# Kernel tuning notes

Measured on AMD Instinct MI355X. Metric: run time of the kernel, lower is better.

Reference implementation:

```python
import jax, jax.numpy as jnp
import numpy as np

B, T, D, H = 2, 2048, 1024, 16  # batch, seq, n_embed, n_head


def setup_inputs() -> dict:
    key = jax.random.key(0)
    ks = jax.random.split(key, 5)
    scale = 1.0 / np.sqrt(D)
    return {
        "x": jax.random.normal(ks[0], (B, T, D), dtype=jnp.float32),
        "Wq": jax.random.normal(ks[1], (D, D), dtype=jnp.float32) * scale,
        "Wk": jax.random.normal(ks[2], (D, D), dtype=jnp.float32) * scale,
        "Wv": jax.random.normal(ks[3], (D, D), dtype=jnp.float32) * scale,
        "Wo": jax.random.normal(ks[4], (D, D), dtype=jnp.float32) * scale,
    }


def reference(x, Wq, Wk, Wv, Wo):
    b, t, d = x.shape
    hd = d // H  # head_dim
    # projections -> [B, H, T, hd]
    q = (x @ Wq).reshape(b, t, H, hd).transpose(0, 2, 1, 3)
    k = (x @ Wk).reshape(b, t, H, hd).transpose(0, 2, 1, 3)
    v = (x @ Wv).reshape(b, t, H, hd).transpose(0, 2, 1, 3)
    # scaled scores [B, H, T, T] with causal mask
    e = jnp.einsum("bhqd,bhkd->bhqk", q, k) * (1.0 / np.sqrt(hd))
    causal = jnp.tril(jnp.ones((t, t), dtype=bool))
    e = jnp.where(causal[None, None], e, jnp.finfo(e.dtype).min)
    alpha = jax.nn.softmax(e, axis=-1)
    # attention output -> [B, T, D]
    attn = jnp.einsum("bhqk,bhkd->bhqd", alpha, v)
    attn = attn.transpose(0, 2, 1, 3).reshape(b, t, d)
    return attn @ Wo
```

## Files before the change

### kernel.cpp

```cpp
#include <hip/hip_runtime.h>
#include <hip/hip_bf16.h>
#include <math.h>


#define Bsz  2
#define Tseq 2048
#define Dm   1024
#define NH   16
#define HD   64

typedef short bf16x8 __attribute__((ext_vector_type(8)));
typedef float floatx4 __attribute__((ext_vector_type(4)));

__device__ __forceinline__ unsigned short f2bf(float f) {
    __hip_bfloat16 h = __float2bfloat16(f);
    return *reinterpret_cast<unsigned short*>(&h);
}

__device__ __forceinline__ unsigned short f2bf_fast(float f) {
    unsigned int u = __builtin_bit_cast(unsigned int, f);
    return (unsigned short)((u + 0x8000u) >> 16);
}

__device__ __forceinline__ void lds16(unsigned short* lds, const unsigned short* g) {
    __builtin_amdgcn_global_load_lds(
        (const __attribute__((address_space(1))) void*)g,
        (__attribute__((address_space(3))) void*)lds, 16, 0, 0);
}

__global__ __launch_bounds__(256) void prep(const float* __restrict__ x,
                                            const float* __restrict__ W0,
                                            const float* __restrict__ W1,
                                            const float* __restrict__ W2,
                                            const float* __restrict__ W3,
                                            unsigned short* __restrict__ xb,
                                            unsigned short* __restrict__ T0,
                                            unsigned short* __restrict__ T1,
                                            unsigned short* __restrict__ T2,
                                            unsigned short* __restrict__ T3) {
    __shared__ float t[64][65];
    const int z = blockIdx.z;
    if (z >= 4) {
        const int bi = (z - 4) * 256 + blockIdx.y * 16 + blockIdx.x;
        const size_t i = (size_t)bi * 256 + threadIdx.x;
        const float4 v = ((const float4*)x)[i];
        ushort4 o;
        o.x = f2bf(v.x); o.y = f2bf(v.y); o.z = f2bf(v.z); o.w = f2bf(v.w);
        ((ushort4*)xb)[i] = o;
        return;
    }
    const float* W = (z == 0) ? W0 : (z == 1) ? W1 : (z == 2) ? W2 : W3;
    unsigned short* T = (z == 0) ? T0 : (z == 1) ? T1 : (z == 2) ? T2 : T3;
    const int k0 = blockIdx.y * 64, n0 = blockIdx.x * 64;
    const int row = threadIdx.x >> 6, col = threadIdx.x & 63;
#pragma unroll
    for (int p = 0; p < 16; ++p)
        t[p * 4 + row][col] = W[(size_t)(k0 + p * 4 + row) * Dm + n0 + col];
    __syncthreads();
#pragma unroll
    for (int p = 0; p < 16; ++p)
        T[(size_t)(n0 + p * 4 + row) * Dm + k0 + col] = f2bf(t[col][p * 4 + row]);
}

__device__ __forceinline__ void gemm128_mainloop(const unsigned short* __restrict__ A,
                                                 const unsigned short* __restrict__ Bt,
                                                 int K, int m0, int n0,
                                                 unsigned short* As, unsigned short* Bs,
                                                 floatx4 acc[4][4]) {
    const int tid = threadIdx.x;
    const int lane = tid & 63, wave = tid >> 6;
    const int l15 = lane & 15, quad = lane >> 4;
    const int wm = (wave >> 1) * 64, wn = (wave & 1) * 64;

    const int qsw = (quad ^ ((l15 >> 1) & 3)) * 8;

    for (int k0 = 0; k0 < K; k0 += 32) {
        __syncthreads();
#pragma unroll
        for (int c = 0; c < 2; ++c) {
            const int idx = c * 256 + tid;
            const int row = idx >> 2, kc = (idx & 3) * 8;
            const int sk = ((idx & 3) ^ ((row >> 1) & 3)) * 8;
            lds16(&As[row * 32 + kc], A + (size_t)(m0 + row) * K + k0 + sk);
            lds16(&Bs[row * 32 + kc], Bt + (size_t)(n0 + row) * K + k0 + sk);
        }
        __syncthreads();
        bf16x8 af[4], bfr[4];
#pragma unroll
        for (int i = 0; i < 4; ++i)
            af[i] = *(const bf16x8*)&As[(wm + i * 16 + l15) * 32 + qsw];
#pragma unroll
        for (int j = 0; j < 4; ++j)
            bfr[j] = *(const bf16x8*)&Bs[(wn + j * 16 + l15) * 32 + qsw];
#pragma unroll
        for (int i = 0; i < 4; ++i)
#pragma unroll
            for (int j = 0; j < 4; ++j)
                acc[i][j] = __builtin_amdgcn_mfma_f32_16x16x32_bf16(af[i], bfr[j], acc[i][j], 0, 0, 0);
    }
}

__global__ __launch_bounds__(256) void gemm_qkv(const unsigned short* __restrict__ xb,
                                                const unsigned short* __restrict__ Wqt,
                                                const unsigned short* __restrict__ Wkt,
                                                const unsigned short* __restrict__ Wvt,
                                                unsigned short* __restrict__ Qb,
                                                unsigned short* __restrict__ Kb,
                                                unsigned short* __restrict__ VbT) {
    __shared__ unsigned short As[128 * 32];
    __shared__ unsigned short Bs[128 * 32];
    const int z = blockIdx.z;
    const unsigned short* Bt = (z == 0) ? Wqt : (z == 1) ? Wkt : Wvt;
    const float scale = (z == 0) ? (0.125f * 1.4426950408889634f) : 1.0f;
    const int m0 = blockIdx.y * 128, n0 = blockIdx.x * 128;

    floatx4 acc[4][4];
#pragma unroll
    for (int i = 0; i < 4; ++i)
#pragma unroll
        for (int j = 0; j < 4; ++j) acc[i][j] = (floatx4){0.f, 0.f, 0.f, 0.f};

    gemm128_mainloop(xb, Bt, Dm, m0, n0, As, Bs, acc);

    const int lane = threadIdx.x & 63, wave = threadIdx.x >> 6;
    const int l15 = lane & 15, quad = lane >> 4;
    const int wm = (wave >> 1) * 64, wn = (wave & 1) * 64;

    if (z == 2) {
#pragma unroll
        for (int i = 0; i < 4; ++i)
#pragma unroll
            for (int j = 0; j < 4; ++j) {
                const int col = n0 + wn + j * 16 + l15;
                const int hh = col >> 6, dd = col & 63;
                const int tok = m0 + wm + i * 16 + quad * 4;
                const int bb = tok >> 11, tl = tok & (Tseq - 1);
                ushort4 o;
                o.x = f2bf(acc[i][j][0]); o.y = f2bf(acc[i][j][1]);
                o.z = f2bf(acc[i][j][2]); o.w = f2bf(acc[i][j][3]);
                *(ushort4*)&VbT[((size_t)((bb * NH + hh) * HD + dd)) * Tseq + tl] = o;
            }
        return;
    }
    unsigned short* C = (z == 0) ? Qb : Kb;
#pragma unroll
    for (int i = 0; i < 4; ++i)
#pragma unroll
        for (int j = 0; j < 4; ++j)
#pragma unroll
            for (int r = 0; r < 4; ++r) {
                const int row = m0 + wm + i * 16 + quad * 4 + r;
                const int col = n0 + wn + j * 16 + l15;
                C[(size_t)row * Dm + col] = f2bf(acc[i][j][r] * scale);
            }
}

__global__ __launch_bounds__(256) void gemm_out(const unsigned short* __restrict__ Yb,
                                                const unsigned short* __restrict__ Wot,
                                                float* __restrict__ out) {
    __shared__ unsigned short As[128 * 32];
    __shared__ unsigned short Bs[64 * 32];
    const int m0 = blockIdx.y * 128, n0 = blockIdx.x * 64;
    const int tid = threadIdx.x;
    const int lane = tid & 63, wave = tid >> 6;
    const int l15 = lane & 15, quad = lane >> 4;
    const int wm = (wave >> 1) * 64, wn = (wave & 1) * 32;
    const int qsw = (quad ^ ((l15 >> 1) & 3)) * 8;

    floatx4 acc[4][2];
#pragma unroll
    for (int i = 0; i < 4; ++i)
#pragma unroll
        for (int j = 0; j < 2; ++j) acc[i][j] = (floatx4){0.f, 0.f, 0.f, 0.f};

    for (int k0 = 0; k0 < Dm; k0 += 32) {
        __syncthreads();
#pragma unroll
        for (int c = 0; c < 2; ++c) {
            const int idx = c * 256 + tid;
            const int row = idx >> 2, kc = (idx & 3) * 8;
            const int sk = ((idx & 3) ^ ((row >> 1) & 3)) * 8;
            lds16(&As[row * 32 + kc], Yb + (size_t)(m0 + row) * Dm + k0 + sk);
        }
        {
            const int row = tid >> 2, kc = (tid & 3) * 8;
            const int sk = ((tid & 3) ^ ((row >> 1) & 3)) * 8;
            lds16(&Bs[row * 32 + kc], Wot + (size_t)(n0 + row) * Dm + k0 + sk);
        }
        __syncthreads();
        bf16x8 af[4], bfr[2];
#pragma unroll
        for (int i = 0; i < 4; ++i)
            af[i] = *(const bf16x8*)&As[(wm + i * 16 + l15) * 32 + qsw];
#pragma unroll
        for (int j = 0; j < 2; ++j)
            bfr[j] = *(const bf16x8*)&Bs[(wn + j * 16 + l15) * 32 + qsw];
#pragma unroll
        for (int i = 0; i < 4; ++i)
#pragma unroll
            for (int j = 0; j < 2; ++j)
                acc[i][j] = __builtin_amdgcn_mfma_f32_16x16x32_bf16(af[i], bfr[j], acc[i][j], 0, 0, 0);
    }

#pragma unroll
    for (int i = 0; i < 4; ++i)
#pragma unroll
        for (int j = 0; j < 2; ++j)
#pragma unroll
            for (int r = 0; r < 4; ++r) {
                const int row = m0 + wm + i * 16 + quad * 4 + r;
                const int col = n0 + wn + j * 16 + l15;
                out[(size_t)row * Dm + col] = acc[i][j][r];
            }
}

__global__ __launch_bounds__(256) void attn_mfma(const unsigned short* __restrict__ Qb,
                                                 const unsigned short* __restrict__ Kb,
                                                 const unsigned short* __restrict__ VbT,
                                                 unsigned short* __restrict__ Yb) {
    const int bh = blockIdx.x;
    const int b = bh >> 4;
    const int h = bh & 15;
    const int qt = 31 - blockIdx.y;
    const int tid = threadIdx.x;
    const int wave = tid >> 6;
    const int lane = tid & 63;
    const int l15 = lane & 15;
    const int quad = lane >> 4;

    __shared__ unsigned short Ks0[2][2][64][32];
    __shared__ unsigned short Ks1[2][2][64][32];
    __shared__ unsigned short Vt0[2][2][64][32];
    __shared__ unsigned short Vt1[2][2][64][32];
    __shared__ unsigned short Ps[4][16][72];

    const size_t tok0 = (size_t)b * Tseq;
    const int colh = h * HD;
    const unsigned short* vbase = VbT + (size_t)bh * HD * Tseq;

    const int qrow = qt * 64 + wave * 16;

    const unsigned short* qptr = Qb + (tok0 + qrow + l15) * Dm + colh + quad * 8;
    const bf16x8 qf0 = *(const bf16x8*)(qptr);
    const bf16x8 qf1 = *(const bf16x8*)(qptr + 32);

    float l_lane = 0.f;
    floatx4 o_acc[4];
#pragma unroll
    for (int t = 0; t < 4; ++t) o_acc[t] = (floatx4){0.f, 0.f, 0.f, 0.f};

    const int srow = tid >> 2;
    const int sc8 = (tid & 3) * 8;
    const int ssw = ((tid & 3) ^ ((srow >> 1) & 3)) * 8;
    const int qsw = (quad ^ ((l15 >> 1) & 3)) * 8;

    const int niter = (qt + 2) >> 1;

    {
        const unsigned short* krow0 = Kb + (tok0 + srow) * Dm + colh;
        const unsigned short* krow1 = Kb + (tok0 + 64 + srow) * Dm + colh;
        const unsigned short* vrow = vbase + (size_t)srow * Tseq;
        lds16(&Ks0[0][0][srow][sc8], krow0 + ssw);
        lds16(&Ks1[0][0][srow][sc8], krow0 + 32 + ssw);
        lds16(&Vt0[0][0][srow][sc8], vrow + ssw);
        lds16(&Vt1[0][0][srow][sc8], vrow + 32 + ssw);
        lds16(&Ks0[0][1][srow][sc8], krow1 + ssw);
        lds16(&Ks1[0][1][srow][sc8], krow1 + 32 + ssw);
        lds16(&Vt0[0][1][srow][sc8], vrow + 64 + ssw);
        lds16(&Vt1[0][1][srow][sc8], vrow + 64 + 32 + ssw);
    }
    asm volatile("s_waitcnt vmcnt(0)" ::: "memory");
    __builtin_amdgcn_s_barrier();
    __builtin_amdgcn_sched_barrier(0);

    for (int it = 0; it < niter; ++it) {
        const int k0 = it * 128;
        const int bi = it & 1;

        if (it + 1 < niter) {
            const int kn = k0 + 128;
#pragma unroll
            for (int s = 0; s < 2; ++s) {
                const unsigned short* krow = Kb + (tok0 + kn + s * 64 + srow) * Dm + colh;
                const unsigned short* vrow = vbase + (size_t)srow * Tseq + kn + s * 64;
                lds16(&Ks0[bi ^ 1][s][srow][sc8], krow + ssw);
                lds16(&Ks1[bi ^ 1][s][srow][sc8], krow + 32 + ssw);
                lds16(&Vt0[bi ^ 1][s][srow][sc8], vrow + ssw);
                lds16(&Vt1[bi ^ 1][s][srow][sc8], vrow + 32 + ssw);
            }
        }
        __builtin_amdgcn_sched_barrier(0);

#pragma unroll
        for (int s = 0; s < 2; ++s) {
            const int k0s = k0 + s * 64;
            if (k0s > qrow + 15) continue;

            floatx4 sf[4];
            __builtin_amdgcn_s_setprio(1);
#pragma unroll
            for (int t = 0; t < 4; ++t) {
                floatx4 c = (floatx4){0.f, 0.f, 0.f, 0.f};
                const bf16x8 kb0 = *(const bf16x8*)&Ks0[bi][s][t * 16 + l15][qsw];
                const bf16x8 kb1 = *(const bf16x8*)&Ks1[bi][s][t * 16 + l15][qsw];
                c = __builtin_amdgcn_mfma_f32_16x16x32_bf16(kb0, qf0, c, 0, 0, 0);
                c = __builtin_amdgcn_mfma_f32_16x16x32_bf16(kb1, qf1, c, 0, 0, 0);
                sf[t] = c;
            }
            __builtin_amdgcn_s_setprio(0);

            if (k0s + 63 > qrow) {
                const int ql = qrow + l15;
#pragma unroll
                for (int t = 0; t < 4; ++t)
#pragma unroll
                    for (int r = 0; r < 4; ++r) {
                        const int kl = k0s + t * 16 + quad * 4 + r;
                        if (kl > ql) sf[t][r] = -1.0e30f;
                    }
            }

#pragma unroll
            for (int t = 0; t < 4; ++t) {
                float p0 = __builtin_amdgcn_exp2f(sf[t][0]);
                float p1 = __builtin_amdgcn_exp2f(sf[t][1]);
                float p2 = __builtin_amdgcn_exp2f(sf[t][2]);
                float p3 = __builtin_amdgcn_exp2f(sf[t][3]);
                l_lane += (p0 + p1) + (p2 + p3);
                unsigned int w0, w1;
                asm("v_cvt_pk_bf16_f32 %0, %1, %2" : "=v"(w0) : "v"(p0), "v"(p1));
                asm("v_cvt_pk_bf16_f32 %0, %1, %2" : "=v"(w1) : "v"(p2), "v"(p3));
                uint2 o; o.x = w0; o.y = w1;
                *(uint2*)&Ps[wave][l15][t * 16 + quad * 4] = o;
            }

            const bf16x8 pa0 = *(const bf16x8*)&Ps[wave][l15][quad * 8];
            const bf16x8 pa1 = *(const bf16x8*)&Ps[wave][l15][32 + quad * 8];
            __builtin_amdgcn_s_setprio(1);
#pragma unroll
            for (int t = 0; t < 4; ++t) {
                const bf16x8 vb0 = *(const bf16x8*)&Vt0[bi][s][t * 16 + l15][qsw];
                const bf16x8 vb1 = *(const bf16x8*)&Vt1[bi][s][t * 16 + l15][qsw];
                o_acc[t] = __builtin_amdgcn_mfma_f32_16x16x32_bf16(pa0, vb0, o_acc[t], 0, 0, 0);
                o_acc[t] = __builtin_amdgcn_mfma_f32_16x16x32_bf16(pa1, vb1, o_acc[t], 0, 0, 0);
            }
            __builtin_amdgcn_s_setprio(0);
        }

        asm volatile("s_waitcnt vmcnt(0)" ::: "memory");
        __builtin_amdgcn_s_barrier();
        __builtin_amdgcn_sched_barrier(0);
    }

    l_lane += __shfl_xor(l_lane, 16);
    l_lane += __shfl_xor(l_lane, 32);
    const float inv_q = 1.0f / l_lane;
    float inv_r[4];
#pragma unroll
    for (int r = 0; r < 4; ++r)
        inv_r[r] = __shfl(inv_q, (lane & 48) | (quad * 4 + r));
#pragma unroll
    for (int t = 0; t < 4; ++t)
#pragma unroll
        for (int r = 0; r < 4; ++r) {
            const int q = qrow + quad * 4 + r;
            Yb[(tok0 + q) * Dm + colh + t * 16 + l15] = f2bf(o_acc[t][r] * inv_r[r]);
        }
}

extern "C" void kernel_launch(void* const* d_in, const int* in_sizes, int n_in,
                              void* d_out, int out_size, void* d_ws, size_t ws_size,
                              hipStream_t stream) {
    const float* x  = (const float*)d_in[0];
    const float* Wq = (const float*)d_in[1];
    const float* Wk = (const float*)d_in[2];
    const float* Wv = (const float*)d_in[3];
    const float* Wo = (const float*)d_in[4];
    float* out = (float*)d_out;

    const int M = Bsz * Tseq;
    char* ws = (char*)d_ws;
    unsigned short* xb  = (unsigned short*)(ws);
    unsigned short* Wqt = (unsigned short*)(ws + (((size_t)8)  << 20));
    unsigned short* Wkt = (unsigned short*)(ws + (((size_t)10) << 20));
    unsigned short* Wvt = (unsigned short*)(ws + (((size_t)12) << 20));
    unsigned short* Wot = (unsigned short*)(ws + (((size_t)14) << 20));
    unsigned short* Qb  = (unsigned short*)(ws + (((size_t)16) << 20));
    unsigned short* Kb  = (unsigned short*)(ws + (((size_t)24) << 20));
    unsigned short* VbT = (unsigned short*)(ws + (((size_t)32) << 20));
    unsigned short* Yb  = (unsigned short*)(ws + (((size_t)40) << 20));

    dim3 blk(256);
    hipLaunchKernelGGL(prep, dim3(16, 16, 20), blk, 0, stream,
                       x, Wq, Wk, Wv, Wo, xb, Wqt, Wkt, Wvt, Wot);

    hipLaunchKernelGGL(gemm_qkv, dim3(Dm / 128, M / 128, 3), blk, 0, stream,
                       xb, Wqt, Wkt, Wvt, Qb, Kb, VbT);

    hipLaunchKernelGGL(attn_mfma, dim3(Bsz * NH, 32), blk, 0, stream, Qb, Kb, VbT, Yb);

    hipLaunchKernelGGL(gemm_out, dim3(Dm / 64, M / 128), blk, 0, stream, Yb, Wot, out);
}
```

Before: 171.8 us.

## Remap GEMM tile order and simplify attention to single-buffered 64-key tiles

```diff
diff --git a/kernel.cpp b/kernel.cpp
--- a/kernel.cpp
+++ b/kernel.cpp
@@ -112,7 +112,11 @@
     const int z = blockIdx.z;
     const unsigned short* Bt = (z == 0) ? Wqt : (z == 1) ? Wkt : Wvt;
     const float scale = (z == 0) ? (0.125f * 1.4426950408889634f) : 1.0f;
-    const int m0 = blockIdx.y * 128, n0 = blockIdx.x * 128;
+
+    const int wg = blockIdx.x + 8 * blockIdx.y;
+    const int m_idx = (wg & 7) * 4 + (wg >> 6);
+    const int n_idx = (wg >> 3) & 7;
+    const int m0 = m_idx * 128, n0 = n_idx * 128;
 
     floatx4 acc[4][4];
 #pragma unroll
@@ -160,7 +164,10 @@
                                                 float* __restrict__ out) {
     __shared__ unsigned short As[128 * 32];
     __shared__ unsigned short Bs[64 * 32];
-    const int m0 = blockIdx.y * 128, n0 = blockIdx.x * 64;
+    const int wg = blockIdx.x + 16 * blockIdx.y;
+    const int m_idx = (wg & 7) * 4 + (wg >> 7);
+    const int n_idx = (wg >> 3) & 15;
+    const int m0 = m_idx * 128, n0 = n_idx * 64;
     const int tid = threadIdx.x;
     const int lane = tid & 63, wave = tid >> 6;
     const int l15 = lane & 15, quad = lane >> 4;
@@ -228,15 +235,14 @@
     const int l15 = lane & 15;
     const int quad = lane >> 4;
 
-    __shared__ unsigned short Ks0[2][2][64][32];
-    __shared__ unsigned short Ks1[2][2][64][32];
-    __shared__ unsigned short Vt0[2][2][64][32];
-    __shared__ unsigned short Vt1[2][2][64][32];
+    __shared__ unsigned short Ks0[64][32];
+    __shared__ unsigned short Ks1[64][32];
+    __shared__ unsigned short Vt0[64][32];
+    __shared__ unsigned short Vt1[64][32];
     __shared__ unsigned short Ps[4][16][72];
 
     const size_t tok0 = (size_t)b * Tseq;
     const int colh = h * HD;
-    const unsigned short* vbase = VbT + (size_t)bh * HD * Tseq;
 
     const int qrow = qt * 64 + wave * 16;
 
@@ -254,102 +260,70 @@
     const int ssw = ((tid & 3) ^ ((srow >> 1) & 3)) * 8;
     const int qsw = (quad ^ ((l15 >> 1) & 3)) * 8;
 
-    const int niter = (qt + 2) >> 1;
-
-    {
-        const unsigned short* krow0 = Kb + (tok0 + srow) * Dm + colh;
-        const unsigned short* krow1 = Kb + (tok0 + 64 + srow) * Dm + colh;
-        const unsigned short* vrow = vbase + (size_t)srow * Tseq;
-        lds16(&Ks0[0][0][srow][sc8], krow0 + ssw);
-        lds16(&Ks1[0][0][srow][sc8], krow0 + 32 + ssw);
-        lds16(&Vt0[0][0][srow][sc8], vrow + ssw);
-        lds16(&Vt1[0][0][srow][sc8], vrow + 32 + ssw);
-        lds16(&Ks0[0][1][srow][sc8], krow1 + ssw);
-        lds16(&Ks1[0][1][srow][sc8], krow1 + 32 + ssw);
-        lds16(&Vt0[0][1][srow][sc8], vrow + 64 + ssw);
-        lds16(&Vt1[0][1][srow][sc8], vrow + 64 + 32 + ssw);
-    }
-    asm volatile("s_waitcnt vmcnt(0)" ::: "memory");
-    __builtin_amdgcn_s_barrier();
-    __builtin_amdgcn_sched_barrier(0);
-
+    const unsigned short* krow = Kb + (tok0 + srow) * Dm + colh;
+    const unsigned short* vrow = VbT + (size_t)bh * HD * Tseq + (size_t)srow * Tseq;
+
+    const int niter = qt + 1;
     for (int it = 0; it < niter; ++it) {
-        const int k0 = it * 128;
-        const int bi = it & 1;
-
-        if (it + 1 < niter) {
-            const int kn = k0 + 128;
-#pragma unroll
-            for (int s = 0; s < 2; ++s) {
-                const unsigned short* krow = Kb + (tok0 + kn + s * 64 + srow) * Dm + colh;
-                const unsigned short* vrow = vbase + (size_t)srow * Tseq + kn + s * 64;
-                lds16(&Ks0[bi ^ 1][s][srow][sc8], krow + ssw);
-                lds16(&Ks1[bi ^ 1][s][srow][sc8], krow + 32 + ssw);
-                lds16(&Vt0[bi ^ 1][s][srow][sc8], vrow + ssw);
-                lds16(&Vt1[bi ^ 1][s][srow][sc8], vrow + 32 + ssw);
-            }
-        }
-        __builtin_amdgcn_sched_barrier(0);
-
-#pragma unroll
-        for (int s = 0; s < 2; ++s) {
-            const int k0s = k0 + s * 64;
-            if (k0s > qrow + 15) continue;
-
-            floatx4 sf[4];
-            __builtin_amdgcn_s_setprio(1);
-#pragma unroll
-            for (int t = 0; t < 4; ++t) {
-                floatx4 c = (floatx4){0.f, 0.f, 0.f, 0.f};
-                const bf16x8 kb0 = *(const bf16x8*)&Ks0[bi][s][t * 16 + l15][qsw];
-                const bf16x8 kb1 = *(const bf16x8*)&Ks1[bi][s][t * 16 + l15][qsw];
-                c = __builtin_amdgcn_mfma_f32_16x16x32_bf16(kb0, qf0, c, 0, 0, 0);
-                c = __builtin_amdgcn_mfma_f32_16x16x32_bf16(kb1, qf1, c, 0, 0, 0);
-                sf[t] = c;
-            }
-            __builtin_amdgcn_s_setprio(0);
-
-            if (k0s + 63 > qrow) {
-                const int ql = qrow + l15;
-#pragma unroll
-                for (int t = 0; t < 4; ++t)
-#pragma unroll
-                    for (int r = 0; r < 4; ++r) {
-                        const int kl = k0s + t * 16 + quad * 4 + r;
-                        if (kl > ql) sf[t][r] = -1.0e30f;
-                    }
-            }
-
-#pragma unroll
-            for (int t = 0; t < 4; ++t) {
-                float p0 = __builtin_amdgcn_exp2f(sf[t][0]);
-                float p1 = __builtin_amdgcn_exp2f(sf[t][1]);
-                float p2 = __builtin_amdgcn_exp2f(sf[t][2]);
-                float p3 = __builtin_amdgcn_exp2f(sf[t][3]);
-                l_lane += (p0 + p1) + (p2 + p3);
-                unsigned int w0, w1;
-                asm("v_cvt_pk_bf16_f32 %0, %1, %2" : "=v"(w0) : "v"(p0), "v"(p1));
-                asm("v_cvt_pk_bf16_f32 %0, %1, %2" : "=v"(w1) : "v"(p2), "v"(p3));
-                uint2 o; o.x = w0; o.y = w1;
-                *(uint2*)&Ps[wave][l15][t * 16 + quad * 4] = o;
-            }
-
-            const bf16x8 pa0 = *(const bf16x8*)&Ps[wave][l15][quad * 8];
-            const bf16x8 pa1 = *(const bf16x8*)&Ps[wave][l15][32 + quad * 8];
-            __builtin_amdgcn_s_setprio(1);
-#pragma unroll
-            for (int t = 0; t < 4; ++t) {
-                const bf16x8 vb0 = *(const bf16x8*)&Vt0[bi][s][t * 16 + l15][qsw];
-                const bf16x8 vb1 = *(const bf16x8*)&Vt1[bi][s][t * 16 + l15][qsw];
-                o_acc[t] = __builtin_amdgcn_mfma_f32_16x16x32_bf16(pa0, vb0, o_acc[t], 0, 0, 0);
-                o_acc[t] = __builtin_amdgcn_mfma_f32_16x16x32_bf16(pa1, vb1, o_acc[t], 0, 0, 0);
-            }
-            __builtin_amdgcn_s_setprio(0);
-        }
-
-        asm volatile("s_waitcnt vmcnt(0)" ::: "memory");
-        __builtin_amdgcn_s_barrier();
-        __builtin_amdgcn_sched_barrier(0);
+        const int k0 = it * 64;
+        __syncthreads();
+        lds16(&Ks0[srow][sc8], krow + ssw);
+        lds16(&Ks1[srow][sc8], krow + 32 + ssw);
+        lds16(&Vt0[srow][sc8], vrow + ssw);
+        lds16(&Vt1[srow][sc8], vrow + 32 + ssw);
+        krow += 64 * Dm;
+        vrow += 64;
+        __syncthreads();
+
+        floatx4 sf[4];
+        __builtin_amdgcn_s_setprio(1);
+#pragma unroll
+        for (int t = 0; t < 4; ++t) {
+            floatx4 c = (floatx4){0.f, 0.f, 0.f, 0.f};
+            const bf16x8 kb0 = *(const bf16x8*)&Ks0[t * 16 + l15][qsw];
+            const bf16x8 kb1 = *(const bf16x8*)&Ks1[t * 16 + l15][qsw];
+            c = __builtin_amdgcn_mfma_f32_16x16x32_bf16(kb0, qf0, c, 0, 0, 0);
+            c = __builtin_amdgcn_mfma_f32_16x16x32_bf16(kb1, qf1, c, 0, 0, 0);
+            sf[t] = c;
+        }
+        __builtin_amdgcn_s_setprio(0);
+
+        if (k0 + 63 > qrow) {
+            const int ql = qrow + l15;
+#pragma unroll
+            for (int t = 0; t < 4; ++t)
+#pragma unroll
+                for (int r = 0; r < 4; ++r) {
+                    const int kl = k0 + t * 16 + quad * 4 + r;
+                    if (kl > ql) sf[t][r] = -1.0e30f;
+                }
+        }
+
+#pragma unroll
+        for (int t = 0; t < 4; ++t) {
+            float p0 = __builtin_amdgcn_exp2f(sf[t][0]);
+            float p1 = __builtin_amdgcn_exp2f(sf[t][1]);
+            float p2 = __builtin_amdgcn_exp2f(sf[t][2]);
+            float p3 = __builtin_amdgcn_exp2f(sf[t][3]);
+            l_lane += (p0 + p1) + (p2 + p3);
+            unsigned int w0, w1;
+            asm("v_cvt_pk_bf16_f32 %0, %1, %2" : "=v"(w0) : "v"(p0), "v"(p1));
+            asm("v_cvt_pk_bf16_f32 %0, %1, %2" : "=v"(w1) : "v"(p2), "v"(p3));
+            uint2 o; o.x = w0; o.y = w1;
+            *(uint2*)&Ps[wave][l15][t * 16 + quad * 4] = o;
+        }
+
+        const bf16x8 pa0 = *(const bf16x8*)&Ps[wave][l15][quad * 8];
+        const bf16x8 pa1 = *(const bf16x8*)&Ps[wave][l15][32 + quad * 8];
+        __builtin_amdgcn_s_setprio(1);
+#pragma unroll
+        for (int t = 0; t < 4; ++t) {
+            const bf16x8 vb0 = *(const bf16x8*)&Vt0[t * 16 + l15][qsw];
+            const bf16x8 vb1 = *(const bf16x8*)&Vt1[t * 16 + l15][qsw];
+            o_acc[t] = __builtin_amdgcn_mfma_f32_16x16x32_bf16(pa0, vb0, o_acc[t], 0, 0, 0);
+            o_acc[t] = __builtin_amdgcn_mfma_f32_16x16x32_bf16(pa1, vb1, o_acc[t], 0, 0, 0);
+        }
+        __builtin_amdgcn_s_setprio(0);
     }
 
     l_lane += __shfl_xor(l_lane, 16);
```

After: 169.1 us. Within noise of the previous version (-1.6%).
